# Kernel optimization log

Hardware: AMD Instinct MI355X
Metric: run time of the kernel (lower is better)

## Reference

```python
import jax, jax.numpy as jnp
import numpy as np

N_NODES = 100000
N_EDGES = 1600000
D_IN = 128
CH = [128, 128]
N_GRAPHS = 256


def _glorot(key, shape):
    lim = float(np.sqrt(6.0 / (shape[0] + shape[1])))
    return jax.random.uniform(key, shape, jnp.float32, -lim, lim)


def setup_inputs() -> dict:
    key = jax.random.key(0)
    ks = jax.random.split(key, 12)
    x = jax.random.normal(ks[0], (N_NODES, D_IN), jnp.float32)
    edge_index = jax.random.randint(ks[1], (2, N_EDGES), 0, N_NODES, jnp.int64)
    batch = jnp.sort(jax.random.randint(ks[2], (N_NODES,), 0, N_GRAPHS, jnp.int64))
    W1 = _glorot(ks[3], (D_IN, CH[0]))
    b1 = jnp.zeros((CH[0],), jnp.float32)
    W2 = _glorot(ks[4], (CH[0], CH[1]))
    b2 = jnp.zeros((CH[1],), jnp.float32)
    Wm1 = _glorot(ks[5], (CH[1], 500)); bm1 = jnp.zeros((500,), jnp.float32)
    Wm2 = _glorot(ks[6], (500, 100));   bm2 = jnp.zeros((100,), jnp.float32)
    Wm3 = _glorot(ks[7], (100, 1));     bm3 = jnp.zeros((1,), jnp.float32)
    return {"x": x, "edge_index": edge_index, "batch": batch,
            "W1": W1, "b1": b1, "W2": W2, "b2": b2,
            "Wm1": Wm1, "bm1": bm1, "Wm2": Wm2, "bm2": bm2,
            "Wm3": Wm3, "bm3": bm3}


def gcn_conv(x, W, b, src, dst, n_nodes):
    # GCNConv with add_self_loops=True, symmetric normalization.
    h = x @ W  # [N, C]
    deg = jnp.zeros((n_nodes,), h.dtype).at[dst].add(1.0) + 1.0  # +1 self loop
    dinv = jax.lax.rsqrt(deg)  # deg >= 1
    norm = dinv[src] * dinv[dst]  # [E]
    agg = jnp.zeros_like(h).at[dst].add(h[src] * norm[:, None])
    agg = agg + h * (dinv * dinv)[:, None]  # self-loop term, norm = dinv[i]^2
    return agg + b


def global_mean_pool(x, batch, n_graphs):
    s = jax.ops.segment_sum(x, batch, num_segments=n_graphs)
    cnt = jax.ops.segment_sum(jnp.ones((x.shape[0],), x.dtype), batch, num_segments=n_graphs)
    return s / jnp.maximum(cnt, 1.0)[:, None]


def reference(x, edge_index, batch, W1, b1, W2, b2, Wm1, bm1, Wm2, bm2, Wm3, bm3):
    src, dst = edge_index[0], edge_index[1]
    h = jax.nn.relu(gcn_conv(x, W1, b1, src, dst, N_NODES))
    h = jax.nn.relu(gcn_conv(h, W2, b2, src, dst, N_NODES))
    g = global_mean_pool(h, batch, N_GRAPHS)  # [G, CH1]
    g = jax.nn.relu(g @ Wm1 + bm1)
    g = jax.nn.relu(g @ Wm2 + bm2)
    return g @ Wm3 + bm3  # [G, 1]
```

## Files before the change

kernel.cpp:

```cpp
#include <hip/hip_runtime.h>

#define CDIM 128
#define NGRAPH 256
#define BSH 7
#define BCAP 4096
#define NBLK 256

typedef unsigned short bf16_t;
typedef __attribute__((ext_vector_type(8))) short bf16x8;
typedef __attribute__((ext_vector_type(4))) float f32x4;

__device__ __forceinline__ float bflo(unsigned u) { return __uint_as_float(u << 16); }
__device__ __forceinline__ float bfhi(unsigned u) { return __uint_as_float(u & 0xffff0000u); }
__device__ __forceinline__ unsigned short f2bf(float f) {
  unsigned u = __float_as_uint(f);
  u += 0x7fffu + ((u >> 16) & 1u);
  return (unsigned short)(u >> 16);
}

__global__ __launch_bounds__(1024) void k_phist(const int* __restrict__ dst,
    int* __restrict__ phist, const float* __restrict__ W1,
    const float* __restrict__ W2, bf16_t* __restrict__ Wtg1,
    bf16_t* __restrict__ Wtg2, float* __restrict__ gb, bf16_t* __restrict__ tz,
    int N, int E, int NB) {
  __shared__ int hist[1024];
  int t = blockIdx.x, tid = threadIdx.x;
  int gidx = t * 1024 + tid;
  if (gidx < 16384) {
    int n = gidx >> 7, k = gidx & 127;
    Wtg1[n * 128 + k] = f2bf(W1[k * 128 + n]);
    Wtg2[n * 128 + k] = f2bf(W2[k * 128 + n]);
  }
  if (gidx < NGRAPH * CDIM) gb[gidx] = 0.f;
  if (gidx < 64) ((unsigned*)(tz + (size_t)N * CDIM))[gidx] = 0u;
  for (int i = tid; i < NB; i += 1024) hist[i] = 0;
  __syncthreads();
  int tile = (E + NBLK - 1) / NBLK;
  int lo = t * tile;
  int hi = lo + tile; if (hi > E) hi = E;
  for (int i = lo + tid; i < hi; i += 1024) atomicAdd(&hist[dst[i] >> BSH], 1);
  __syncthreads();
  for (int i = tid; i < NB; i += 1024) phist[i * NBLK + t] = hist[i];
}

__global__ __launch_bounds__(256) void k_bscan(int* __restrict__ phist,
    int* __restrict__ btot) {
  __shared__ int wsum[4];
  int b = blockIdx.x;
  int tid = threadIdx.x, lane = tid & 63, wave = tid >> 6;
  int orig = phist[b * NBLK + tid];
  int v = orig;
#pragma unroll
  for (int ofs = 1; ofs < 64; ofs <<= 1) {
    int u = __shfl_up(v, ofs, 64);
    if (lane >= ofs) v += u;
  }
  if (lane == 63) wsum[wave] = v;
  __syncthreads();
  int add = 0;
#pragma unroll
  for (int w = 0; w < 3; w++) if (w < wave) add += wsum[w];
  int incl = v + add;
  phist[b * NBLK + tid] = incl - orig;
  if (tid == 255) btot[b] = incl;
}

__global__ __launch_bounds__(1024) void k_boff(const int* __restrict__ bsums,
    int* __restrict__ boffs, int G) {
  __shared__ int sh[1024];
  int tid = threadIdx.x;
  int v = (tid < G) ? bsums[tid] : 0;
  sh[tid] = v;
  __syncthreads();
  for (int ofs = 1; ofs < 1024; ofs <<= 1) {
    int u = (tid >= ofs) ? sh[tid - ofs] : 0;
    __syncthreads();
    sh[tid] += u;
    __syncthreads();
  }
  if (tid < G) boffs[tid] = sh[tid] - v;
  if (tid == G) boffs[G] = (G > 0) ? sh[G - 1] : 0;
}

__global__ __launch_bounds__(1024) void k_pscatter(const int* __restrict__ src,
    const int* __restrict__ dst, const int* __restrict__ phist,
    const int* __restrict__ bbase, unsigned* __restrict__ tmp, int E, int NB) {
  __shared__ int cur[1024];
  int t = blockIdx.x, tid = threadIdx.x;
  for (int i = tid; i < NB; i += 1024) cur[i] = bbase[i] + phist[i * NBLK + t];
  __syncthreads();
  int tile = (E + NBLK - 1) / NBLK;
  int lo = t * tile;
  int hi = lo + tile; if (hi > E) hi = E;
  for (int i = lo + tid; i < hi; i += 1024) {
    int d = dst[i];
    int p = atomicAdd(&cur[d >> BSH], 1);
    tmp[p] = (unsigned)src[i] | ((unsigned)(d & 127) << 20);
  }
}

__global__ __launch_bounds__(256) void k_csort2(const unsigned* __restrict__ tmp,
    const int* __restrict__ bbase, int* __restrict__ rowptr, float* __restrict__ dinv,
    int* __restrict__ col, int N, int NB, int E) {
  __shared__ int hist[128];
  __shared__ int sc[128];
  __shared__ int lcur[128];
  __shared__ unsigned buf[BCAP];
  int b = blockIdx.x;
  int n0 = b << BSH;
  int base = bbase[b];
  int cnt = bbase[b + 1] - base;
  int tid = threadIdx.x;
  if (tid < 128) hist[tid] = 0;
  __syncthreads();
  for (int i = tid; i < cnt; i += 256) atomicAdd(&hist[(tmp[base + i] >> 20) & 127], 1);
  __syncthreads();
  if (tid < 128) sc[tid] = hist[tid];
  __syncthreads();
  for (int ofs = 1; ofs < 128; ofs <<= 1) {
    int v = (tid < 128 && tid >= ofs) ? sc[tid - ofs] : 0;
    __syncthreads();
    if (tid < 128) sc[tid] += v;
    __syncthreads();
  }
  if (tid < 128) {
    int excl = sc[tid] - hist[tid];
    lcur[tid] = excl;
    int node = n0 + tid;
    if (node < N) {
      rowptr[node] = base + excl;
      dinv[node] = rsqrtf((float)hist[tid] + 1.0f);
    }
  }
  if (b == 0 && tid == 0) rowptr[N] = E;
  __syncthreads();
  if (cnt <= BCAP) {
    for (int i = tid; i < cnt; i += 256) {
      unsigned pk = tmp[base + i];
      int p = atomicAdd(&lcur[(pk >> 20) & 127], 1);
      buf[p] = pk & 0xFFFFFu;
    }
    __syncthreads();
    for (int i = tid; i < cnt; i += 256) col[base + i] = (int)buf[i];
  } else {
    for (int i = tid; i < cnt; i += 256) {
      unsigned pk = tmp[base + i];
      int p = atomicAdd(&lcur[(pk >> 20) & 127], 1);
      col[base + p] = (int)(pk & 0xFFFFFu);
    }
  }
}

#define WSTRIDE 136
template <int BF16IN>
__global__ __launch_bounds__(256) void k_gemm(const void* __restrict__ Ap,
    const bf16_t* __restrict__ Wtg, const float* __restrict__ dscale,
    bf16_t* __restrict__ Co, int M) {
  __shared__ bf16_t Wt[128 * WSTRIDE];
  int tid = threadIdx.x;
  for (int c2 = tid; c2 < 2048; c2 += 256) {
    int n = c2 >> 4;
    int k8 = (c2 & 15) << 3;
    *(uint4*)&Wt[n * WSTRIDE + k8] = *(const uint4*)&Wtg[n * 128 + k8];
  }
  __syncthreads();

  int wave = tid >> 6;
  int lane = tid & 63;
  int m = lane & 15;
  int q = lane >> 4;
  int nstrips = (M + 63) >> 6;

  for (int s = blockIdx.x; s < nstrips; s += gridDim.x) {
    int rowA = s * 64 + wave * 16 + m;
    if (rowA > M - 1) rowA = M - 1;
    bf16x8 a[4];
#pragma unroll
    for (int c = 0; c < 4; c++) {
      if (BF16IN) {
        a[c] = *(const bf16x8*)((const bf16_t*)Ap + (size_t)rowA * CDIM + c * 32 + q * 8);
      } else {
        const float* ap = (const float*)Ap + (size_t)rowA * CDIM + c * 32 + q * 8;
        float4 f0 = *(const float4*)ap;
        float4 f1 = *(const float4*)(ap + 4);
        union { bf16x8 v; unsigned short u[8]; } ua;
        ua.u[0] = f2bf(f0.x); ua.u[1] = f2bf(f0.y); ua.u[2] = f2bf(f0.z); ua.u[3] = f2bf(f0.w);
        ua.u[4] = f2bf(f1.x); ua.u[5] = f2bf(f1.y); ua.u[6] = f2bf(f1.z); ua.u[7] = f2bf(f1.w);
        a[c] = ua.v;
      }
    }
    float sc[4];
#pragma unroll
    for (int r = 0; r < 4; r++) {
      int row = s * 64 + wave * 16 + q * 4 + r;
      sc[r] = (row < M) ? dscale[row] : 0.f;
    }
#pragma unroll
    for (int t = 0; t < 8; t++) {
      f32x4 acc = {0.f, 0.f, 0.f, 0.f};
#pragma unroll
      for (int c = 0; c < 4; c++) {
        bf16x8 bv = *(const bf16x8*)&Wt[(t * 16 + m) * WSTRIDE + c * 32 + q * 8];
        acc = __builtin_amdgcn_mfma_f32_16x16x32_bf16(a[c], bv, acc, 0, 0, 0);
      }
#pragma unroll
      for (int r = 0; r < 4; r++) {
        int row = s * 64 + wave * 16 + q * 4 + r;
        if (row < M) Co[(size_t)row * CDIM + t * 16 + m] = f2bf(acc[r] * sc[r]);
      }
    }
  }
}

#define GISS(S, V, JJ) \
  { _Pragma("unroll") for (int u = 0; u < 8; u++) \
      S[u] = __builtin_amdgcn_readlane(sL, (JJ) + u); \
    _Pragma("unroll") for (int u = 0; u < 8; u++) \
      V[u] = tp[(size_t)S[u] * 64 + lane]; }
#define GCON(V) \
  { _Pragma("unroll") for (int u = 0; u < 8; u++) { \
      a0 += bflo(V[u]); a1 += bfhi(V[u]); } }
#define GBLOCK(CNT) \
  { int nb = ((CNT) + 7) >> 3; \
    GISS(sA, vA, 0); \
    int b_ = 1; \
    for (; b_ + 1 < nb; b_ += 2) { \
      GISS(sB, vB, b_ * 8);       GCON(vA); \
      GISS(sA, vA, (b_ + 1) * 8); GCON(vB); \
    } \
    if (b_ < nb) { GISS(sB, vB, b_ * 8); GCON(vA); GCON(vB); } \
    else { GCON(vA); } }

__global__ __launch_bounds__(256) void k_agg0(const bf16_t* __restrict__ t,
    const int* __restrict__ rowptr, const int* __restrict__ col,
    const float* __restrict__ dinv, const float* __restrict__ bias,
    bf16_t* __restrict__ out, int N) {
  int wave = threadIdx.x >> 6;
  int lane = threadIdx.x & 63;
  int node = blockIdx.x * 4 + wave;
  if (node >= N) return;
  const unsigned* tp = (const unsigned*)t;
  float di = dinv[node];
  unsigned sv = tp[(size_t)node * 64 + lane];
  float a0 = bflo(sv);
  float a1 = bfhi(sv);
  int beg = rowptr[node], end = rowptr[node + 1];
  int sA[8]; unsigned vA[8];
  int sB[8]; unsigned vB[8];
  for (int base = beg; base < end; base += 64) {
    int cnt = end - base; if (cnt > 64) cnt = 64;
    int sL = N;
    if (lane < cnt) sL = col[base + lane];
    GBLOCK(cnt);
  }
  float2 bb = ((const float2*)bias)[lane];
  float o0 = fmaxf(fmaf(di, a0, bb.x), 0.f);
  float o1 = fmaxf(fmaf(di, a1, bb.y), 0.f);
  ((unsigned*)out)[(size_t)node * 64 + lane] =
      ((unsigned)f2bf(o1) << 16) | f2bf(o0);
}

__global__ __launch_bounds__(256) void k_aggp(const bf16_t* __restrict__ t,
    const int* __restrict__ rowptr, const int* __restrict__ col,
    const float* __restrict__ dinv, const float* __restrict__ bias,
    const int* __restrict__ batch, float* __restrict__ gsum, int N) {
  int wave = threadIdx.x >> 6;
  int lane = threadIdx.x & 63;
  int n0 = (blockIdx.x * 4 + wave) * 16;
  if (n0 >= N) return;
  int nEnd = n0 + 16; if (nEnd > N) nEnd = N;
  const unsigned* tp = (const unsigned*)t;
  float2 bb = ((const float2*)bias)[lane];
  float p0 = 0.f, p1 = 0.f;
  int curb = batch[n0];
  int sA[8]; unsigned vA[8];
  int sB[8]; unsigned vB[8];

  for (int node = n0; node < nEnd; node++) {
    float di = dinv[node];
    unsigned sv = tp[(size_t)node * 64 + lane];
    float a0 = bflo(sv);
    float a1 = bfhi(sv);
    int beg = rowptr[node], end = rowptr[node + 1];
    for (int base = beg; base < end; base += 64) {
      int cnt = end - base; if (cnt > 64) cnt = 64;
      int sL = N;
      if (lane < cnt) sL = col[base + lane];
      GBLOCK(cnt);
    }
    float o0 = fmaxf(fmaf(di, a0, bb.x), 0.f);
    float o1 = fmaxf(fmaf(di, a1, bb.y), 0.f);
    int b = batch[node];
    if (b != curb) {
      atomicAdd(&gsum[curb * CDIM + 2 * lane], p0);
      atomicAdd(&gsum[curb * CDIM + 2 * lane + 1], p1);
      curb = b; p0 = p1 = 0.f;
    }
    p0 += __uint_as_float((unsigned)f2bf(o0) << 16);
    p1 += __uint_as_float((unsigned)f2bf(o1) << 16);
  }
  atomicAdd(&gsum[curb * CDIM + 2 * lane], p0);
  atomicAdd(&gsum[curb * CDIM + 2 * lane + 1], p1);
}

__global__ __launch_bounds__(512) void k_mlp(const float* __restrict__ g,
    const int* __restrict__ batch, int N,
    const float* __restrict__ Wm1, const float* __restrict__ bm1,
    const float* __restrict__ Wm2, const float* __restrict__ bm2,
    const float* __restrict__ wm3, const float* __restrict__ bm3,
    float* __restrict__ out) {
  __shared__ float gs[CDIM];
  __shared__ float m1s[500];
  __shared__ float m2s[100];
  int bi = blockIdx.x, tid = threadIdx.x;
  if (tid < CDIM) {
    int lo = 0, hi = N;
    while (lo < hi) { int mid = (lo + hi) >> 1; if (batch[mid] < bi) lo = mid + 1; else hi = mid; }
    int s = lo;
    lo = 0; hi = N;
    int key = bi + 1;
    while (lo < hi) { int mid = (lo + hi) >> 1; if (batch[mid] < key) lo = mid + 1; else hi = mid; }
    float inv = 1.f / fmaxf((float)(lo - s), 1.f);
    gs[tid] = g[bi * CDIM + tid] * inv;
  }
  __syncthreads();
  if (tid < 500) {
    float acc = bm1[tid];
#pragma unroll 4
    for (int k = 0; k < CDIM; k++) acc = fmaf(gs[k], Wm1[k * 500 + tid], acc);
    m1s[tid] = fmaxf(acc, 0.f);
  }
  __syncthreads();
  if (tid < 100) {
    float acc = bm2[tid];
    for (int k = 0; k < 500; k++) acc = fmaf(m1s[k], Wm2[k * 100 + tid], acc);
    m2s[tid] = fmaxf(acc, 0.f) * wm3[tid];
  }
  __syncthreads();
  if (tid < 64) {
    float v = m2s[tid] + ((tid + 64 < 100) ? m2s[tid + 64] : 0.f);
#pragma unroll
    for (int ofs = 32; ofs > 0; ofs >>= 1) v += __shfl_down(v, ofs, 64);
    if (tid == 0) out[bi] = v + bm3[0];
  }
}

static inline size_t align_up(size_t v) { return (v + 255) & ~(size_t)255; }

extern "C" void kernel_launch(void* const* d_in, const int* in_sizes, int n_in,
                              void* d_out, int out_size, void* d_ws, size_t ws_size,
                              hipStream_t stream) {
  const float* x   = (const float*)d_in[0];
  const int*   ei  = (const int*)d_in[1];
  const int*   bat = (const int*)d_in[2];
  const float* W1  = (const float*)d_in[3];
  const float* b1  = (const float*)d_in[4];
  const float* W2  = (const float*)d_in[5];
  const float* b2  = (const float*)d_in[6];
  const float* Wm1 = (const float*)d_in[7];
  const float* bm1 = (const float*)d_in[8];
  const float* Wm2 = (const float*)d_in[9];
  const float* bm2 = (const float*)d_in[10];
  const float* Wm3 = (const float*)d_in[11];
  const float* bm3 = (const float*)d_in[12];
  float* out = (float*)d_out;

  const int E = in_sizes[1] / 2;
  const int N = in_sizes[2];
  const int* src = ei;
  const int* dst = ei + E;
  const int NB = (N + 127) >> BSH;
  const int M  = NB * NBLK;

  char* p = (char*)d_ws;
  bf16_t* t    = (bf16_t*)p;   p += align_up((size_t)(N + 1) * CDIM * 2);
  bf16_t* h    = (bf16_t*)p;   p += align_up((size_t)N * CDIM * 2);
  int* rowptr  = (int*)p;      p += align_up((size_t)(N + 1) * 4);
  int* colx    = (int*)p;      p += align_up((size_t)E * 4);
  unsigned* tmp= (unsigned*)p; p += align_up((size_t)E * 4);
  float* dinv  = (float*)p;    p += align_up((size_t)N * 4);
  int* phist   = (int*)p;      p += align_up((size_t)M * 4);
  int* btot    = (int*)p;      p += align_up((size_t)NB * 4);
  int* bbase   = (int*)p;      p += align_up((size_t)(NB + 1) * 4);
  bf16_t* Wtg1 = (bf16_t*)p;   p += align_up((size_t)CDIM * CDIM * 2);
  bf16_t* Wtg2 = (bf16_t*)p;   p += align_up((size_t)CDIM * CDIM * 2);
  float* gb    = (float*)p;    p += align_up((size_t)NGRAPH * CDIM * 4);
  (void)ws_size; (void)n_in; (void)out_size;

  k_phist<<<NBLK, 1024, 0, stream>>>(dst, phist, W1, W2, Wtg1, Wtg2, gb, t, N, E, NB);
  k_bscan<<<NB, 256, 0, stream>>>(phist, btot);
  k_boff<<<1, 1024, 0, stream>>>(btot, bbase, NB);
  k_pscatter<<<NBLK, 1024, 0, stream>>>(src, dst, phist, bbase, tmp, E, NB);
  k_csort2<<<NB, 256, 0, stream>>>(tmp, bbase, rowptr, dinv, colx, N, NB, E);

  k_gemm<0><<<512, 256, 0, stream>>>(x, Wtg1, dinv, t, N);
  k_agg0<<<(N + 3) / 4, 256, 0, stream>>>(t, rowptr, colx, dinv, b1, h, N);
  k_gemm<1><<<512, 256, 0, stream>>>(h, Wtg2, dinv, t, N);
  int pwaves = (N + 15) / 16;
  k_aggp<<<(pwaves + 3) / 4, 256, 0, stream>>>(t, rowptr, colx, dinv, b2,
                                               bat, gb, N);
  k_mlp<<<NGRAPH, 512, 0, stream>>>(gb, bat, N, Wm1, bm1, Wm2, bm2, Wm3, bm3, out);
}
```

Before: 328.2 us.

## Fuse layer-1 aggregation with layer-2 GEMM and fold bucket offset scan

The layer-1 aggregation now runs in 1024-thread blocks that gather 64 nodes into shared memory and immediately multiply them by W2 with MFMA. This removes the separate k_gemm<1> launch and the global round trip of the intermediate h tensor. The k_boff kernel is also removed: the bucket offset scan is recomputed inside k_pscatter, and each k_csort2 block reduces its own prefix. Pooling waves drop from 16 to 8 nodes each for more parallelism. In exchange, every csort2 block does a redundant reduction, and the fused kernel has lower occupancy because of its large shared memory footprint and block size.

```diff
diff --git a/kernel.cpp b/kernel.cpp
--- a/kernel.cpp
+++ b/kernel.cpp
@@ -21,8 +21,8 @@
 __global__ __launch_bounds__(1024) void k_phist(const int* __restrict__ dst,
     int* __restrict__ phist, const float* __restrict__ W1,
     const float* __restrict__ W2, bf16_t* __restrict__ Wtg1,
-    bf16_t* __restrict__ Wtg2, float* __restrict__ gb, bf16_t* __restrict__ tz,
-    int N, int E, int NB) {
+    bf16_t* __restrict__ Wtg2, float* __restrict__ gb, bf16_t* __restrict__ tz1,
+    bf16_t* __restrict__ tz2, int N, int E, int NB) {
   __shared__ int hist[1024];
   int t = blockIdx.x, tid = threadIdx.x;
   int gidx = t * 1024 + tid;
@@ -32,7 +32,10 @@
     Wtg2[n * 128 + k] = f2bf(W2[k * 128 + n]);
   }
   if (gidx < NGRAPH * CDIM) gb[gidx] = 0.f;
-  if (gidx < 64) ((unsigned*)(tz + (size_t)N * CDIM))[gidx] = 0u;
+  if (gidx < 64) {
+    ((unsigned*)(tz1 + (size_t)N * CDIM))[gidx] = 0u;
+    ((unsigned*)(tz2 + (size_t)N * CDIM))[gidx] = 0u;
+  }
   for (int i = tid; i < NB; i += 1024) hist[i] = 0;
   __syncthreads();
   int tile = (E + NBLK - 1) / NBLK;
@@ -65,11 +68,13 @@
   if (tid == 255) btot[b] = incl;
 }
 
-__global__ __launch_bounds__(1024) void k_boff(const int* __restrict__ bsums,
-    int* __restrict__ boffs, int G) {
+__global__ __launch_bounds__(1024) void k_pscatter(const int* __restrict__ src,
+    const int* __restrict__ dst, const int* __restrict__ phist,
+    const int* __restrict__ btot, unsigned* __restrict__ tmp, int E, int NB) {
+  __shared__ int cur[1024];
   __shared__ int sh[1024];
-  int tid = threadIdx.x;
-  int v = (tid < G) ? bsums[tid] : 0;
+  int t = blockIdx.x, tid = threadIdx.x;
+  int v = (tid < NB) ? btot[tid] : 0;
   sh[tid] = v;
   __syncthreads();
   for (int ofs = 1; ofs < 1024; ofs <<= 1) {
@@ -78,16 +83,7 @@
     sh[tid] += u;
     __syncthreads();
   }
-  if (tid < G) boffs[tid] = sh[tid] - v;
-  if (tid == G) boffs[G] = (G > 0) ? sh[G - 1] : 0;
-}
-
-__global__ __launch_bounds__(1024) void k_pscatter(const int* __restrict__ src,
-    const int* __restrict__ dst, const int* __restrict__ phist,
-    const int* __restrict__ bbase, unsigned* __restrict__ tmp, int E, int NB) {
-  __shared__ int cur[1024];
-  int t = blockIdx.x, tid = threadIdx.x;
-  for (int i = tid; i < NB; i += 1024) cur[i] = bbase[i] + phist[i * NBLK + t];
+  if (tid < NB) cur[tid] = (sh[tid] - v) + phist[tid * NBLK + t];
   __syncthreads();
   int tile = (E + NBLK - 1) / NBLK;
   int lo = t * tile;
@@ -100,17 +96,26 @@
 }
 
 __global__ __launch_bounds__(256) void k_csort2(const unsigned* __restrict__ tmp,
-    const int* __restrict__ bbase, int* __restrict__ rowptr, float* __restrict__ dinv,
+    const int* __restrict__ btot, int* __restrict__ rowptr, float* __restrict__ dinv,
     int* __restrict__ col, int N, int NB, int E) {
   __shared__ int hist[128];
   __shared__ int sc[128];
   __shared__ int lcur[128];
+  __shared__ int red[256];
   __shared__ unsigned buf[BCAP];
   int b = blockIdx.x;
   int n0 = b << BSH;
-  int base = bbase[b];
-  int cnt = bbase[b + 1] - base;
   int tid = threadIdx.x;
+  int part = 0;
+  for (int j = tid; j < b; j += 256) part += btot[j];
+  red[tid] = part;
+  __syncthreads();
+  for (int ofs = 128; ofs > 0; ofs >>= 1) {
+    if (tid < ofs) red[tid] += red[tid + ofs];
+    __syncthreads();
+  }
+  int base = red[0];
+  int cnt = btot[b];
   if (tid < 128) hist[tid] = 0;
   __syncthreads();
   for (int i = tid; i < cnt; i += 256) atomicAdd(&hist[(tmp[base + i] >> 20) & 127], 1);
@@ -231,33 +236,72 @@
     if (b_ < nb) { GISS(sB, vB, b_ * 8); GCON(vA); GCON(vB); } \
     else { GCON(vA); } }
 
-__global__ __launch_bounds__(256) void k_agg0(const bf16_t* __restrict__ t,
+__global__ __launch_bounds__(1024) void k_aggg(const bf16_t* __restrict__ t,
     const int* __restrict__ rowptr, const int* __restrict__ col,
     const float* __restrict__ dinv, const float* __restrict__ bias,
-    bf16_t* __restrict__ out, int N) {
-  int wave = threadIdx.x >> 6;
-  int lane = threadIdx.x & 63;
-  int node = blockIdx.x * 4 + wave;
-  if (node >= N) return;
+    const bf16_t* __restrict__ Wtg, bf16_t* __restrict__ to, int N) {
+  __shared__ bf16_t Wt[128 * WSTRIDE];
+  __shared__ unsigned hs[64 * 68];
+  int tid = threadIdx.x;
+  int wave = tid >> 6, lane = tid & 63;
+  for (int c2 = tid; c2 < 2048; c2 += 1024) {
+    int n = c2 >> 4, k8 = (c2 & 15) << 3;
+    *(uint4*)&Wt[n * WSTRIDE + k8] = *(const uint4*)&Wtg[n * 128 + k8];
+  }
   const unsigned* tp = (const unsigned*)t;
-  float di = dinv[node];
-  unsigned sv = tp[(size_t)node * 64 + lane];
-  float a0 = bflo(sv);
-  float a1 = bfhi(sv);
-  int beg = rowptr[node], end = rowptr[node + 1];
+  float2 bb = ((const float2*)bias)[lane];
   int sA[8]; unsigned vA[8];
   int sB[8]; unsigned vB[8];
-  for (int base = beg; base < end; base += 64) {
-    int cnt = end - base; if (cnt > 64) cnt = 64;
-    int sL = N;
-    if (lane < cnt) sL = col[base + lane];
-    GBLOCK(cnt);
-  }
-  float2 bb = ((const float2*)bias)[lane];
-  float o0 = fmaxf(fmaf(di, a0, bb.x), 0.f);
-  float o1 = fmaxf(fmaf(di, a1, bb.y), 0.f);
-  ((unsigned*)out)[(size_t)node * 64 + lane] =
-      ((unsigned)f2bf(o1) << 16) | f2bf(o0);
+  int nbase = blockIdx.x * 64;
+#pragma unroll 1
+  for (int i = 0; i < 4; i++) {
+    int node = nbase + wave * 4 + i;
+    unsigned hv = 0u;
+    if (node < N) {
+      float di = dinv[node];
+      unsigned sv = tp[(size_t)node * 64 + lane];
+      float a0 = bflo(sv), a1 = bfhi(sv);
+      int beg = rowptr[node], end = rowptr[node + 1];
+      for (int base = beg; base < end; base += 64) {
+        int cnt = end - base; if (cnt > 64) cnt = 64;
+        int sL = N;
+        if (lane < cnt) sL = col[base + lane];
+        GBLOCK(cnt);
+      }
+      float o0 = fmaxf(fmaf(di, a0, bb.x), 0.f);
+      float o1 = fmaxf(fmaf(di, a1, bb.y), 0.f);
+      hv = ((unsigned)f2bf(o1) << 16) | f2bf(o0);
+    }
+    hs[(wave * 4 + i) * 68 + lane] = hv;
+  }
+  __syncthreads();
+  int rg = wave & 3, cg = wave >> 2;
+  int m = lane & 15, q = lane >> 4;
+  bf16x8 a[4];
+#pragma unroll
+  for (int c = 0; c < 4; c++)
+    a[c] = *(const bf16x8*)&hs[(rg * 16 + m) * 68 + c * 16 + q * 4];
+  float sc4[4]; int rows[4];
+#pragma unroll
+  for (int r = 0; r < 4; r++) {
+    int row = nbase + rg * 16 + q * 4 + r;
+    rows[r] = row;
+    sc4[r] = (row < N) ? dinv[row] : 0.f;
+  }
+#pragma unroll
+  for (int tt = 0; tt < 2; tt++) {
+    int tcol = cg * 2 + tt;
+    f32x4 acc = {0.f, 0.f, 0.f, 0.f};
+#pragma unroll
+    for (int c = 0; c < 4; c++) {
+      bf16x8 bv = *(const bf16x8*)&Wt[(tcol * 16 + m) * WSTRIDE + c * 32 + q * 8];
+      acc = __builtin_amdgcn_mfma_f32_16x16x32_bf16(a[c], bv, acc, 0, 0, 0);
+    }
+#pragma unroll
+    for (int r = 0; r < 4; r++)
+      if (rows[r] < N)
+        to[(size_t)rows[r] * CDIM + tcol * 16 + m] = f2bf(acc[r] * sc4[r]);
+  }
 }
 
 __global__ __launch_bounds__(256) void k_aggp(const bf16_t* __restrict__ t,
@@ -266,9 +310,9 @@
     const int* __restrict__ batch, float* __restrict__ gsum, int N) {
   int wave = threadIdx.x >> 6;
   int lane = threadIdx.x & 63;
-  int n0 = (blockIdx.x * 4 + wave) * 16;
+  int n0 = (blockIdx.x * 4 + wave) * 8;
   if (n0 >= N) return;
-  int nEnd = n0 + 16; if (nEnd > N) nEnd = N;
+  int nEnd = n0 + 8; if (nEnd > N) nEnd = N;
   const unsigned* tp = (const unsigned*)t;
   float2 bb = ((const float2*)bias)[lane];
   float p0 = 0.f, p1 = 0.f;
@@ -374,30 +418,26 @@
 
   char* p = (char*)d_ws;
   bf16_t* t    = (bf16_t*)p;   p += align_up((size_t)(N + 1) * CDIM * 2);
-  bf16_t* h    = (bf16_t*)p;   p += align_up((size_t)N * CDIM * 2);
+  bf16_t* t2   = (bf16_t*)p;   p += align_up((size_t)(N + 1) * CDIM * 2);
   int* rowptr  = (int*)p;      p += align_up((size_t)(N + 1) * 4);
   int* colx    = (int*)p;      p += align_up((size_t)E * 4);
   unsigned* tmp= (unsigned*)p; p += align_up((size_t)E * 4);
   float* dinv  = (float*)p;    p += align_up((size_t)N * 4);
   int* phist   = (int*)p;      p += align_up((size_t)M * 4);
   int* btot    = (int*)p;      p += align_up((size_t)NB * 4);
-  int* bbase   = (int*)p;      p += align_up((size_t)(NB + 1) * 4);
   bf16_t* Wtg1 = (bf16_t*)p;   p += align_up((size_t)CDIM * CDIM * 2);
   bf16_t* Wtg2 = (bf16_t*)p;   p += align_up((size_t)CDIM * CDIM * 2);
   float* gb    = (float*)p;    p += align_up((size_t)NGRAPH * CDIM * 4);
   (void)ws_size; (void)n_in; (void)out_size;
 
-  k_phist<<<NBLK, 1024, 0, stream>>>(dst, phist, W1, W2, Wtg1, Wtg2, gb, t, N, E, NB);
+  k_phist<<<NBLK, 1024, 0, stream>>>(dst, phist, W1, W2, Wtg1, Wtg2, gb, t, t2, N, E, NB);
   k_bscan<<<NB, 256, 0, stream>>>(phist, btot);
-  k_boff<<<1, 1024, 0, stream>>>(btot, bbase, NB);
-  k_pscatter<<<NBLK, 1024, 0, stream>>>(src, dst, phist, bbase, tmp, E, NB);
-  k_csort2<<<NB, 256, 0, stream>>>(tmp, bbase, rowptr, dinv, colx, N, NB, E);
+  k_pscatter<<<NBLK, 1024, 0, stream>>>(src, dst, phist, btot, tmp, E, NB);
+  k_csort2<<<NB, 256, 0, stream>>>(tmp, btot, rowptr, dinv, colx, N, NB, E);
 
   k_gemm<0><<<512, 256, 0, stream>>>(x, Wtg1, dinv, t, N);
-  k_agg0<<<(N + 3) / 4, 256, 0, stream>>>(t, rowptr, colx, dinv, b1, h, N);
-  k_gemm<1><<<512, 256, 0, stream>>>(h, Wtg2, dinv, t, N);
-  int pwaves = (N + 15) / 16;
-  k_aggp<<<(pwaves + 3) / 4, 256, 0, stream>>>(t, rowptr, colx, dinv, b2,
-                                               bat, gb, N);
+  k_aggg<<<(N + 63) / 64, 1024, 0, stream>>>(t, rowptr, colx, dinv, b1, Wtg2, t2, N);
+  int pw = (N + 7) / 8;
+  k_aggp<<<(pw + 3) / 4, 256, 0, stream>>>(t2, rowptr, colx, dinv, b2, bat, gb, N);
   k_mlp<<<NGRAPH, 512, 0, stream>>>(gb, bat, N, Wm1, bm1, Wm2, bm2, Wm3, bm3, out);
 }
```

New measurement: 327.6 us. About the same (-0.2%).
